# Kernel tuning notes

Hardware: AMD Instinct MI355X
Metric: run time of the kernel (lower is better)

## Reference

```python
import jax, jax.numpy as jnp
import numpy as np

N_NODES = 100000
N_EDGES = 1600000
IN_DIM = 256
OUT_DIM = 64


def setup_inputs() -> dict:
    key = jax.random.key(0)
    k1, k2, k3, k4, k5 = jax.random.split(key, 5)
    h = jax.random.normal(k1, (N_NODES, IN_DIM), dtype=jnp.float32)
    src = jax.random.randint(k2, (N_EDGES,), 0, N_NODES, dtype=jnp.int32)
    dst = jax.random.randint(k3, (N_EDGES,), 0, N_NODES, dtype=jnp.int32)
    # xavier_normal with gain for relu (sqrt(2))
    gain = float(np.sqrt(2.0))
    std_w = gain * float(np.sqrt(2.0 / (IN_DIM + OUT_DIM)))
    W = jax.random.normal(k4, (OUT_DIM, IN_DIM), dtype=jnp.float32) * std_w
    std_a = gain * float(np.sqrt(2.0 / (2 * OUT_DIM + 1)))
    a = jax.random.normal(k5, (2 * OUT_DIM,), dtype=jnp.float32) * std_a
    return {"h": h, "src": src, "dst": dst, "W": W, "a": a}


def reference(h, src, dst, W, a):
    # linear projection: W_h[n, out]
    W_h = h @ W.T
    # edge attention: e = relu(a . concat(W_h[src], W_h[dst]))
    a_src, a_dst = a[:OUT_DIM], a[OUT_DIM:]
    e = jax.nn.relu(W_h[src] @ a_src + W_h[dst] @ a_dst)  # [E]
    # segment softmax over incoming edges of each dst node
    m = jax.ops.segment_max(e, dst, num_segments=N_NODES)  # [N]
    ex = jnp.exp(e - m[dst])
    s = jax.ops.segment_sum(ex, dst, num_segments=N_NODES)  # [N]
    alpha = ex / s[dst]  # [E]
    # weighted scatter-sum of source messages
    h_N = jax.ops.segment_sum(alpha[:, None] * W_h[src], dst, num_segments=N_NODES)
    return h_N
```

## Files before the change

### kernel.cpp

```cpp
#include <hip/hip_runtime.h>
#include <hip/hip_bf16.h>
#include <math.h>
#include <stdint.h>

#define N_NODES 100000
#define N_EDGES 1600000
#define IN_DIM 256
#define OUT_DIM 64

#define CWIN  64
#define NCB   1563
#define NPART 256
#define EPP   (N_EDGES / NPART)
#define EBCAP 1536
#define MAXE  EBCAP

#define GEMM_BLKS ((N_NODES + 255) / 256)


typedef __attribute__((ext_vector_type(8))) short bh8;
typedef __attribute__((ext_vector_type(4))) float f4;

typedef __attribute__((address_space(1))) const void GV;
typedef __attribute__((address_space(3))) void LV;

static __device__ __forceinline__ unsigned short f2bf(float f) {
    unsigned u = __float_as_uint(f);
    unsigned r = (u + 0x7FFFu + ((u >> 16) & 1u)) >> 16;
    return (unsigned short)r;
}

__global__ __launch_bounds__(1024) void gat_mega(
    const float* __restrict__ h, const float* __restrict__ W,
    const float* __restrict__ a, unsigned short* __restrict__ WhB,
    float* __restrict__ p_src, float* __restrict__ p_dst,
    const int* __restrict__ src, const int* __restrict__ dst,
    int* __restrict__ gcur, int* __restrict__ ebufA)
{
    __shared__ __align__(16) unsigned short Wlds[64 * 256];

    const int t = threadIdx.x;

    if (blockIdx.x >= GEMM_BLKS) {
        const int part = blockIdx.x - GEMM_BLKS;
        int* lh   = (int*)Wlds;
        int* lcur = ((int*)Wlds) + NCB;

        for (int i = t; i < NCB; i += 1024) lh[i] = 0;
        __syncthreads();
        const int e0 = part * EPP;
        for (int e = e0 + t; e < e0 + EPP; e += 1024)
            atomicAdd(&lh[dst[e] >> 6], 1);
        __syncthreads();
        for (int i = t; i < NCB; i += 1024) {
            const int c = lh[i];
            lcur[i] = c ? atomicAdd(&gcur[i], c) : 0;
        }
        __syncthreads();
        for (int e = e0 + t; e < e0 + EPP; e += 1024) {
            const int se = src[e], de = dst[e];
            const int w = de >> 6;
            const int off = atomicAdd(&lcur[w], 1);
            ebufA[w * EBCAP + off] = se | ((de & (CWIN - 1)) << 17);
        }
        return;
    }

    const int lane = t & 63;
    const int wv = t >> 6;
    const int cl = lane & 15;
    const int g  = lane >> 4;
    const int node0 = blockIdx.x * 256 + wv * 16;

    #pragma unroll
    for (int cc = 0; cc < 2; ++cc) {
        const int cell = t + cc * 1024;
        const int col = cell & 63;
        const int k16 = cell >> 6;
        const float4 lo = *(const float4*)(W + col * IN_DIM + k16 * 8);
        const float4 hi = *(const float4*)(W + col * IN_DIM + k16 * 8 + 4);
        unsigned short tmp[8];
        tmp[0] = f2bf(lo.x); tmp[1] = f2bf(lo.y);
        tmp[2] = f2bf(lo.z); tmp[3] = f2bf(lo.w);
        tmp[4] = f2bf(hi.x); tmp[5] = f2bf(hi.y);
        tmp[6] = f2bf(hi.z); tmp[7] = f2bf(hi.w);
        *(uint4*)&Wlds[cell * 8] = *(uint4*)tmp;
    }
    __syncthreads();

    int row = node0 + cl;
    row = (row < N_NODES) ? row : N_NODES - 1;
    const float* __restrict__ hp = h + (size_t)row * IN_DIM + g * 8;

    f4 acc[4];
    #pragma unroll
    for (int nt = 0; nt < 4; ++nt) acc[nt] = (f4){0.f, 0.f, 0.f, 0.f};

    #pragma unroll
    for (int j = 0; j < 8; ++j) {
        const float4 lo = *(const float4*)(hp + j * 32);
        const float4 hi = *(const float4*)(hp + j * 32 + 4);
        bh8 af;
        af[0] = (short)f2bf(lo.x); af[1] = (short)f2bf(lo.y);
        af[2] = (short)f2bf(lo.z); af[3] = (short)f2bf(lo.w);
        af[4] = (short)f2bf(hi.x); af[5] = (short)f2bf(hi.y);
        af[6] = (short)f2bf(hi.z); af[7] = (short)f2bf(hi.w);

        #pragma unroll
        for (int nt = 0; nt < 4; ++nt) {
            const bh8 bf = *(const bh8*)&Wlds[(((j * 4 + g) * 64) + nt * 16 + cl) * 8];
            acc[nt] = __builtin_amdgcn_mfma_f32_16x16x32_bf16(af, bf, acc[nt], 0, 0, 0);
        }
    }

    float aS[4], aD[4];
    #pragma unroll
    for (int nt = 0; nt < 4; ++nt) {
        aS[nt] = a[nt * 16 + cl];
        aD[nt] = a[OUT_DIM + nt * 16 + cl];
    }

    #pragma unroll
    for (int r = 0; r < 4; ++r) {
        const int orow = node0 + g * 4 + r;
        float ps = 0.f, pd = 0.f;
        #pragma unroll
        for (int nt = 0; nt < 4; ++nt) {
            ps = fmaf(acc[nt][r], aS[nt], ps);
            pd = fmaf(acc[nt][r], aD[nt], pd);
        }
        #pragma unroll
        for (int o = 8; o > 0; o >>= 1) {
            ps += __shfl_xor(ps, o);
            pd += __shfl_xor(pd, o);
        }
        if (orow < N_NODES) {
            const unsigned lo2 = (unsigned)f2bf(acc[0][r]) |
                                 ((unsigned)f2bf(acc[1][r]) << 16);
            const unsigned hi2 = (unsigned)f2bf(acc[2][r]) |
                                 ((unsigned)f2bf(acc[3][r]) << 16);
            *(uint2*)&WhB[(size_t)orow * OUT_DIM + cl * 4] = make_uint2(lo2, hi2);
            if (cl == 0) { p_src[orow] = ps; p_dst[orow] = pd; }
        }
    }
}

__global__ __launch_bounds__(256) void gat_agg_fused(
    const int* __restrict__ ebufA, const int* __restrict__ gcnt,
    const float* __restrict__ p_src, const float* __restrict__ p_dst,
    const unsigned short* __restrict__ Wh, float* __restrict__ out)
{
    __shared__ int2 ledge[MAXE];
    __shared__ int lhist[CWIN], lbase[CWIN];
    __shared__ float pdl[CWIN];

    const int t = threadIdx.x;
    const int cb = blockIdx.x;
    const int a0 = cb * EBCAP;
    const int cnt = min(gcnt[cb], MAXE);
    const int wbase = cb * CWIN;

    if (t < CWIN) {
        lhist[t] = 0;
        const int node = wbase + t;
        pdl[t] = (node < N_NODES) ? p_dst[node] : 0.f;
    }
    __syncthreads();

    int   ev[6], rk[6];
    float ps[6];
    #pragma unroll
    for (int j = 0; j < 6; ++j) {
        const int i = t + j * 256;
        ev[j] = 0; rk[j] = 0; ps[j] = 0.f;
        if (i < cnt) {
            const int e = ebufA[a0 + i];
            ev[j] = e;
            ps[j] = p_src[e & 0x1FFFF];
            rk[j] = atomicAdd(&lhist[(e >> 17) & (CWIN - 1)], 1);
        }
    }
    __syncthreads();

    if (t < 64) {
        const int own = lhist[t];
        int val = own;
        #pragma unroll
        for (int s = 1; s < 64; s <<= 1) {
            const int n = __shfl_up(val, s);
            if (t >= s) val += n;
        }
        lbase[t] = val - own;
    }
    __syncthreads();

    #pragma unroll
    for (int j = 0; j < 6; ++j) {
        const int i = t + j * 256;
        if (i < cnt) {
            const int e = ev[j];
            const int ln = (e >> 17) & (CWIN - 1);
            const float ex = __expf(fmaxf(ps[j] + pdl[ln], 0.f));
            ledge[lbase[ln] + rk[j]] = make_int2(e & 0x1FFFF, __float_as_int(ex));
        }
    }
    __syncthreads();

    const int lane = t & 63;
    const int wv = t >> 6;
    const int grp = lane >> 4;
    const int ci = lane & 15;
    const int c4 = ci * 4;

    #pragma unroll
    for (int rr = 0; rr < 4; ++rr) {
        const int ln = wv * 16 + rr * 4 + grp;
        const int node = wbase + ln;
        const int sb = lbase[ln];
        const int d  = (node < N_NODES) ? lhist[ln] : 0;

        float ssum = 0.f;
        float a0f = 0.f, a1f = 0.f, a2f = 0.f, a3f = 0.f;

        #pragma unroll 4
        for (int k = 0; k < d; ++k) {
            const int2 ed = ledge[sb + k];
            const float ex = __int_as_float(ed.y);
            const uint2 wr = *(const uint2*)(Wh + (size_t)ed.x * OUT_DIM + c4);
            ssum += ex;
            a0f = fmaf(ex, __uint_as_float(wr.x << 16), a0f);
            a1f = fmaf(ex, __uint_as_float(wr.x & 0xFFFF0000u), a1f);
            a2f = fmaf(ex, __uint_as_float(wr.y << 16), a2f);
            a3f = fmaf(ex, __uint_as_float(wr.y & 0xFFFF0000u), a3f);
        }

        if (node < N_NODES) {
            const float inv = (d > 0) ? 1.f / ssum : 0.f;
            float* ob = out + (size_t)node * OUT_DIM;
            ob[ci]      = a0f * inv;
            ob[16 + ci] = a1f * inv;
            ob[32 + ci] = a2f * inv;
            ob[48 + ci] = a3f * inv;
        }
    }
}

extern "C" void kernel_launch(void* const* d_in, const int* in_sizes, int n_in,
                              void* d_out, int out_size, void* d_ws, size_t ws_size,
                              hipStream_t stream)
{
    const float* h  = (const float*)d_in[0];
    const int* src  = (const int*)d_in[1];
    const int* dst  = (const int*)d_in[2];
    const float* W  = (const float*)d_in[3];
    const float* a  = (const float*)d_in[4];
    float* out = (float*)d_out;

    char* ws = (char*)d_ws;
    unsigned short* WhB = (unsigned short*)(ws);
    float* p_src   = (float*)(ws + 12800000);
    float* p_dst   = (float*)(ws + 13200000);
    int*   gcur    = (int*)  (ws + 13600000);
    int*   ebufA   = (int*)  (ws + 13606252 + 4);

    hipMemsetAsync(gcur, 0, NCB * sizeof(int), stream);
    gat_mega<<<GEMM_BLKS + NPART, 1024, 0, stream>>>(
        h, W, a, WhB, p_src, p_dst, src, dst, gcur, ebufA);
    gat_agg_fused<<<NCB, 256, 0, stream>>>(ebufA, gcur, p_src, p_dst, WhB, out);
}
```

Measured before the change: 85.58 us.

## Pre-pack h and W to bf16 MFMA-fragment layout in a separate kernel

Adds a pack kernel that converts h into bf16 tiles already arranged in MFMA operand order and converts W to bf16. The GEMM kernel then loads these fragments directly and stages W into LDS with global_load_lds instead of converting inline. The goal is to take float-to-bf16 conversion and strided loads off the GEMM path. In exchange it adds a kernel launch and a full extra pass over h (reading 102MB and writing 51MB). It also needs a larger workspace and falls back to the old fp32 path when the workspace is too small.

```diff
diff --git a/kernel.cpp b/kernel.cpp
--- a/kernel.cpp
+++ b/kernel.cpp
@@ -16,6 +16,7 @@
 #define MAXE  EBCAP
 
 #define GEMM_BLKS ((N_NODES + 255) / 256)
+#define NTILE (N_NODES / 16)
 
 
 typedef __attribute__((ext_vector_type(8))) short bh8;
@@ -30,7 +31,156 @@
     return (unsigned short)r;
 }
 
-__global__ __launch_bounds__(1024) void gat_mega(
+__global__ __launch_bounds__(256) void gat_pack(
+    const float* __restrict__ h, unsigned short* __restrict__ hP,
+    const float* __restrict__ W, unsigned short* __restrict__ WB)
+{
+    const int t = threadIdx.x;
+
+    if (blockIdx.x >= NTILE) {
+        const int cell = (blockIdx.x - NTILE) * 256 + t;
+        const int col = cell & 63;
+        const int k16 = cell >> 6;
+        const float4 lo = *(const float4*)(W + col * IN_DIM + k16 * 8);
+        const float4 hi = *(const float4*)(W + col * IN_DIM + k16 * 8 + 4);
+        unsigned short tmp[8];
+        tmp[0] = f2bf(lo.x); tmp[1] = f2bf(lo.y);
+        tmp[2] = f2bf(lo.z); tmp[3] = f2bf(lo.w);
+        tmp[4] = f2bf(hi.x); tmp[5] = f2bf(hi.y);
+        tmp[6] = f2bf(hi.z); tmp[7] = f2bf(hi.w);
+        *(uint4*)&WB[(size_t)cell * 8] = *(uint4*)tmp;
+        return;
+    }
+
+    __shared__ float lds[16 * 260];
+    const size_t base = (size_t)blockIdx.x * 16 * IN_DIM;
+
+    #pragma unroll
+    for (int it = 0; it < 4; ++it) {
+        const int idx = it * 256 + t;
+        const float4 v = *(const float4*)(h + base + (size_t)idx * 4);
+        const int row = idx >> 6;
+        const int coloff = (idx & 63) * 4;
+        *(float4*)&lds[row * 260 + coloff] = v;
+    }
+    __syncthreads();
+
+    #pragma unroll
+    for (int cc = 0; cc < 2; ++cc) {
+        const int c = t + cc * 256;
+        const int cl = c & 15;
+        const int g  = (c >> 4) & 3;
+        const int j  = c >> 6;
+        const float* s = &lds[cl * 260 + j * 32 + g * 8];
+        unsigned short tmp[8];
+        #pragma unroll
+        for (int x = 0; x < 8; ++x) tmp[x] = f2bf(s[x]);
+        *(uint4*)&hP[(size_t)blockIdx.x * 4096 + (size_t)c * 8] = *(uint4*)tmp;
+    }
+}
+
+__global__ __launch_bounds__(1024) void gat_mega_bf(
+    const unsigned short* __restrict__ hP, const unsigned short* __restrict__ WB,
+    const float* __restrict__ a, unsigned short* __restrict__ WhB,
+    float* __restrict__ p_src, float* __restrict__ p_dst,
+    const int* __restrict__ src, const int* __restrict__ dst,
+    int* __restrict__ gcur, int* __restrict__ ebufA)
+{
+    __shared__ __align__(16) unsigned short Wlds[64 * 256];
+
+    const int t = threadIdx.x;
+
+    if (blockIdx.x >= GEMM_BLKS) {
+        const int part = blockIdx.x - GEMM_BLKS;
+        int* lh   = (int*)Wlds;
+        int* lcur = ((int*)Wlds) + NCB;
+
+        for (int i = t; i < NCB; i += 1024) lh[i] = 0;
+        __syncthreads();
+        const int e0 = part * EPP;
+        for (int e = e0 + t; e < e0 + EPP; e += 1024)
+            atomicAdd(&lh[dst[e] >> 6], 1);
+        __syncthreads();
+        for (int i = t; i < NCB; i += 1024) {
+            const int c = lh[i];
+            lcur[i] = c ? atomicAdd(&gcur[i], c) : 0;
+        }
+        __syncthreads();
+        for (int e = e0 + t; e < e0 + EPP; e += 1024) {
+            const int se = src[e], de = dst[e];
+            const int w = de >> 6;
+            const int off = atomicAdd(&lcur[w], 1);
+            ebufA[w * EBCAP + off] = se | ((de & (CWIN - 1)) << 17);
+        }
+        return;
+    }
+
+    const int lane = t & 63;
+    const int wv = t >> 6;
+    const int cl = lane & 15;
+    const int g  = lane >> 4;
+    const int node0 = blockIdx.x * 256 + wv * 16;
+
+    #pragma unroll
+    for (int i = 0; i < 2; ++i) {
+        const int chunk = wv * 2 + i;
+        __builtin_amdgcn_global_load_lds(
+            (GV*)(WB + chunk * 512 + lane * 8),
+            (LV*)(((char*)Wlds) + chunk * 1024), 16, 0, 0);
+    }
+    __syncthreads();
+
+    int T = blockIdx.x * 16 + wv;
+    T = (T < NTILE) ? T : NTILE - 1;
+    const unsigned short* __restrict__ hpw = hP + (size_t)T * 4096;
+
+    f4 acc[4];
+    #pragma unroll
+    for (int nt = 0; nt < 4; ++nt) acc[nt] = (f4){0.f, 0.f, 0.f, 0.f};
+
+    #pragma unroll
+    for (int j = 0; j < 8; ++j) {
+        const bh8 af = *(const bh8*)&hpw[j * 512 + lane * 8];
+        #pragma unroll
+        for (int nt = 0; nt < 4; ++nt) {
+            const bh8 bf = *(const bh8*)&Wlds[(((j * 4 + g) * 64) + nt * 16 + cl) * 8];
+            acc[nt] = __builtin_amdgcn_mfma_f32_16x16x32_bf16(af, bf, acc[nt], 0, 0, 0);
+        }
+    }
+
+    float aS[4], aD[4];
+    #pragma unroll
+    for (int nt = 0; nt < 4; ++nt) {
+        aS[nt] = a[nt * 16 + cl];
+        aD[nt] = a[OUT_DIM + nt * 16 + cl];
+    }
+
+    #pragma unroll
+    for (int r = 0; r < 4; ++r) {
+        const int orow = node0 + g * 4 + r;
+        float ps = 0.f, pd = 0.f;
+        #pragma unroll
+        for (int nt = 0; nt < 4; ++nt) {
+            ps = fmaf(acc[nt][r], aS[nt], ps);
+            pd = fmaf(acc[nt][r], aD[nt], pd);
+        }
+        #pragma unroll
+        for (int o = 8; o > 0; o >>= 1) {
+            ps += __shfl_xor(ps, o);
+            pd += __shfl_xor(pd, o);
+        }
+        if (orow < N_NODES) {
+            const unsigned lo2 = (unsigned)f2bf(acc[0][r]) |
+                                 ((unsigned)f2bf(acc[1][r]) << 16);
+            const unsigned hi2 = (unsigned)f2bf(acc[2][r]) |
+                                 ((unsigned)f2bf(acc[3][r]) << 16);
+            *(uint2*)&WhB[(size_t)orow * OUT_DIM + cl * 4] = make_uint2(lo2, hi2);
+            if (cl == 0) { p_src[orow] = ps; p_dst[orow] = pd; }
+        }
+    }
+}
+
+__global__ __launch_bounds__(1024) void gat_mega_f32(
     const float* __restrict__ h, const float* __restrict__ W,
     const float* __restrict__ a, unsigned short* __restrict__ WhB,
     float* __restrict__ p_src, float* __restrict__ p_dst,
@@ -45,7 +195,6 @@
         const int part = blockIdx.x - GEMM_BLKS;
         int* lh   = (int*)Wlds;
         int* lcur = ((int*)Wlds) + NCB;
-
         for (int i = t; i < NCB; i += 1024) lh[i] = 0;
         __syncthreads();
         const int e0 = part * EPP;
@@ -105,7 +254,6 @@
         af[2] = (short)f2bf(lo.z); af[3] = (short)f2bf(lo.w);
         af[4] = (short)f2bf(hi.x); af[5] = (short)f2bf(hi.y);
         af[6] = (short)f2bf(hi.z); af[7] = (short)f2bf(hi.w);
-
         #pragma unroll
         for (int nt = 0; nt < 4; ++nt) {
             const bh8 bf = *(const bh8*)&Wlds[(((j * 4 + g) * 64) + nt * 16 + cl) * 8];
@@ -261,10 +409,20 @@
     float* p_src   = (float*)(ws + 12800000);
     float* p_dst   = (float*)(ws + 13200000);
     int*   gcur    = (int*)  (ws + 13600000);
-    int*   ebufA   = (int*)  (ws + 13606252 + 4);
+    int*   ebufA   = (int*)  (ws + 13606400);
+    unsigned short* WB = (unsigned short*)(ws + 23209472);
+    unsigned short* hP = (unsigned short*)(ws + 23242240);
+    const size_t NEED = 23242240ull + 51200000ull;
 
     hipMemsetAsync(gcur, 0, NCB * sizeof(int), stream);
-    gat_mega<<<GEMM_BLKS + NPART, 1024, 0, stream>>>(
-        h, W, a, WhB, p_src, p_dst, src, dst, gcur, ebufA);
+
+    if (ws_size >= NEED) {
+        gat_pack<<<NTILE + 8, 256, 0, stream>>>(h, hP, W, WB);
+        gat_mega_bf<<<GEMM_BLKS + NPART, 1024, 0, stream>>>(
+            hP, WB, a, WhB, p_src, p_dst, src, dst, gcur, ebufA);
+    } else {
+        gat_mega_f32<<<GEMM_BLKS + NPART, 1024, 0, stream>>>(
+            h, W, a, WhB, p_src, p_dst, src, dst, gcur, ebufA);
+    }
     gat_agg_fused<<<NCB, 256, 0, stream>>>(ebufA, gcur, p_src, p_dst, WhB, out);
 }
```

Measured after the change: 102.9 us. 20.3% more time.
